# Optimization experiments

Measured on AMD Instinct MI355X. Metric: run time of the kernel, lower is better.

Reference implementation:

```python
import jax, jax.numpy as jnp
import numpy as np
from jax import lax

B, D, N, K, POOL = 256, 512, 50000, 32, 1024
ALPHA, BETA, LAMB = 1.0, 1.0, 1e-4
TAU, EPS, DELTA = 0.1, 0.1, 1e-3
SINKHORN_ITERS = 200


def matrix_sqrt(A):
    # differentiable symmetric PSD matrix sqrt via eigendecomposition
    w, v = jnp.linalg.eigh(A)
    w = jnp.clip(w, 0.0)
    return (v * jnp.sqrt(w)) @ v.T


def ridge_cov(M, delta):
    Dm = M.shape[0]
    S = M + (jnp.trace(M) / Dm * delta) * jnp.eye(Dm, dtype=M.dtype)
    return 0.5 * (S + S.T)


def sinkhorn(p, q, C, eps):
    # entropic OT, fixed-iteration Sinkhorn (ot.sinkhorn equivalent)
    Kmat = jnp.exp(-C / eps)
    def step(uv, _):
        u, v = uv
        u = p / (Kmat @ v + 1e-16)
        v = q / (Kmat.T @ u + 1e-16)
        return (u, v), None
    (u, v), _ = lax.scan(step, (jnp.ones_like(p), jnp.ones_like(q)), None, length=SINKHORN_ITERS)
    return u[:, None] * Kmat * v[None, :]


def setup_inputs():
    key = jax.random.key(0)
    k1, k2, k3, k4, k5, k6 = jax.random.split(key, 6)
    return {
        "q_batch": jax.random.normal(k1, (B, D), jnp.float32),
        "q_indices": jax.random.randint(k2, (B,), 0, POOL),
        "W": jax.random.normal(k3, (D, D), jnp.float32) * 0.05,
        "X": jax.random.normal(k4, (N, D), jnp.float32),
        "pre_indices": jax.random.randint(k5, (POOL, K), 0, N),
        "pre_weights": jax.random.uniform(k6, (POOL, K), jnp.float32, 0.1, 1.0),
    }


def _forward(q_batch, W, X, pre_weights, q_indices, pre_indices):
    T = q_batch @ W  # model := single linear layer, T_q_batch [B, D]
    # ---- distribution alignment (2-Wasserstein between Gaussians) ----
    mu_X = X.mean(0)
    Sigma_X = ridge_cov(jnp.cov(X, rowvar=False).astype(X.dtype), DELTA)
    mu_t = T.mean(0)
    Sigma_t = ridge_cov(jnp.cov(T, rowvar=False).astype(T.dtype), max(DELTA, 1e-4))
    term_mean = jnp.sum((mu_t - mu_X) ** 2)
    s_t = matrix_sqrt(Sigma_t)
    M = s_t @ Sigma_X @ s_t
    s_m = matrix_sqrt(0.5 * (M + M.T))
    term_cov = jnp.trace(Sigma_X + Sigma_t - 2.0 * s_m)
    loss_dist = term_mean + jnp.clip(term_cov, 0.0)
    # ---- kNN consistency with entropic OT ----
    T_sg = lax.stop_gradient(T)  # faiss search is on detached queries
    d2 = (T_sg ** 2).sum(1, keepdims=True) - 2.0 * T_sg @ X.T + (X ** 2).sum(1)[None, :]
    _, post_idx = lax.top_k(-d2, K)  # exact brute-force kNN == faiss IndexFlatL2
    Xn = X[post_idx]  # [B, K, D]
    l2 = ((T[:, None, :] - Xn) ** 2).sum(-1)  # [B, K], grads flow through T
    post_w = jax.nn.softmax(-l2 / TAU, axis=1)
    post_w = jnp.clip(post_w, 1e-8)
    post_w = post_w / post_w.sum(1, keepdims=True)
    pre_idx_b = pre_indices[q_indices]  # [B, K]
    pre_w = jnp.clip(pre_weights[q_indices], 1e-8)
    pre_w = pre_w / pre_w.sum(1, keepdims=True)
    # fixed-size support = concat(pre, post) of size 2K; duplicated points cost 0
    # to move between, so OT value matches the deduped-union formulation
    support = jnp.concatenate([pre_idx_b, post_idx], axis=1)  # [B, 2K]
    S = X[support]  # [B, 2K, D]
    sq = (S ** 2).sum(-1)
    C = jnp.clip(sq[:, :, None] + sq[:, None, :] - 2.0 * jnp.einsum('bid,bjd->bij', S, S), 0.0)
    med = jnp.median(C.reshape(C.shape[0], -1), axis=1)
    C = C / (med[:, None, None] + 1e-8)
    zeros = jnp.zeros_like(pre_w)
    p = jnp.concatenate([pre_w, zeros], axis=1)   # pre mass on first K slots
    q = jnp.concatenate([zeros, post_w], axis=1)  # post mass on last K slots
    plans = jax.vmap(lambda pp, qq, cc: sinkhorn(pp, qq, cc, EPS))(p, q, C)
    loss_knn = (plans * C).sum((1, 2)).mean()
    loss_reg = 0.5 * jnp.sum(W ** 2)
    total = ALPHA * loss_dist + BETA * loss_knn + LAMB * loss_reg
    return total, loss_dist, loss_knn


def reference(q_batch, q_indices, W, X, pre_indices, pre_weights):
    return _forward(q_batch, W, X, pre_weights, q_indices, pre_indices)
```

## Files before the change

### kernel.cpp

```cpp
#include <hip/hip_runtime.h>
#include <float.h>
#include <math.h>

#define BB 256
#define DD 512
#define NN 50000
#define KK 32
#define NS_ITERS 11
#define PARTS 8
#define PCH 6250

#define OFF_G     0
#define OFF_SC    262144
#define OFF_CS    262208
#define OFF_CSS   262720
#define ZERO_F    263232
#define OFF_T     263232
#define OFF_TC    394304
#define OFF_P     525376
#define OFF_H     656448
#define OFF_XSQ   723008
#define OFF_RUNI  781200
#define OFF_PW    789392
#define OFF_PRW   797584
#define OFF_D2    805776

#define OFF_UUT   (OFF_G)
#define OFF_TCTC  (OFF_G + 65536)
#define OFF_W     (OFF_G + 131072)
#define OFF_M     (OFF_G + 131328)
#define OFF_MUT   (OFF_G + 200000)

typedef __attribute__((ext_vector_type(8))) short bf16x8;
typedef __attribute__((ext_vector_type(4))) float f32x4;

__device__ __forceinline__ float waveSum(float v) {
#pragma unroll
  for (int off = 32; off > 0; off >>= 1) v += __shfl_xor(v, off);
  return v;
}

__device__ __forceinline__ void cvt_write(float4 v, unsigned short* hi, unsigned short* lo, int sa) {
  unsigned int b0 = __float_as_uint(v.x), b1 = __float_as_uint(v.y);
  unsigned int b2 = __float_as_uint(v.z), b3 = __float_as_uint(v.w);
  unsigned int h0 = b0 & 0xffff0000u, h1 = b1 & 0xffff0000u;
  unsigned int h2 = b2 & 0xffff0000u, h3 = b3 & 0xffff0000u;
  float l0 = v.x - __uint_as_float(h0), l1 = v.y - __uint_as_float(h1);
  float l2 = v.z - __uint_as_float(h2), l3 = v.w - __uint_as_float(h3);
  *(unsigned int*)&hi[sa]     = (h0 >> 16) | h1;
  *(unsigned int*)&hi[sa + 2] = (h2 >> 16) | h3;
  *(unsigned int*)&lo[sa]     = (__float_as_uint(l0) >> 16) | (__float_as_uint(l1) & 0xffff0000u);
  *(unsigned int*)&lo[sa + 2] = (__float_as_uint(l2) >> 16) | (__float_as_uint(l3) & 0xffff0000u);
}

__device__ __forceinline__ void cvt1(float x, unsigned short* hp, unsigned short* lp) {
  unsigned int bb = __float_as_uint(x);
  unsigned int hb = bb & 0xffff0000u;
  float lo = x - __uint_as_float(hb);
  *hp = (unsigned short)(hb >> 16);
  *lp = (unsigned short)(__float_as_uint(lo) >> 16);
}

__global__ void __launch_bounds__(256) k_g64_nn(const float* __restrict__ A,
                                                const float* __restrict__ B,
                                                float* __restrict__ C,
                                                int K, int lda, int ldb, int ldc, float scale,
                                                float* __restrict__ musum) {
  __shared__ float As[64][65], Bs[64][65];
  __shared__ float cp[64];
  int m0 = blockIdx.y * 64, n0 = blockIdx.x * 64;
  int t = threadIdx.x, tr = t >> 4, tc = t & 15;
  float acc[4][4] = {{0.f}};
  for (int k0 = 0; k0 < K; k0 += 64) {
#pragma unroll
    for (int p = 0; p < 16; ++p) {
      int l = t + 256 * p;
      int r = l >> 6, c = l & 63;
      As[r][c] = A[(m0 + r) * lda + k0 + c];
      Bs[r][c] = B[(k0 + r) * ldb + n0 + c];
    }
    __syncthreads();
#pragma unroll 16
    for (int kk = 0; kk < 64; ++kk) {
      float a[4], b[4];
#pragma unroll
      for (int u = 0; u < 4; ++u) a[u] = As[tr + 16 * u][kk];
#pragma unroll
      for (int v = 0; v < 4; ++v) b[v] = Bs[kk][tc + 16 * v];
#pragma unroll
      for (int u = 0; u < 4; ++u)
#pragma unroll
        for (int v = 0; v < 4; ++v) acc[u][v] += a[u] * b[v];
    }
    __syncthreads();
  }
#pragma unroll
  for (int u = 0; u < 4; ++u)
#pragma unroll
    for (int v = 0; v < 4; ++v)
      C[(m0 + tr + 16 * u) * ldc + n0 + tc + 16 * v] = acc[u][v] * scale;
  if (musum != nullptr) {
    if (t < 64) cp[t] = 0.f;
    __syncthreads();
#pragma unroll
    for (int v = 0; v < 4; ++v) {
      float s = 0.f;
#pragma unroll
      for (int u = 0; u < 4; ++u) s += acc[u][v];
      atomicAdd(&cp[tc + 16 * v], s * scale);
    }
    __syncthreads();
    if (t < 64) atomicAdd(&musum[n0 + t], cp[t]);
  }
}

__global__ void __launch_bounds__(256) k_g64_nt(const float* __restrict__ A,
                                                const float* __restrict__ B,
                                                float* __restrict__ C,
                                                int K, int lda, int ldb, int ldc, float scale) {
  __shared__ float As[64][65], Bs[64][65];
  int m0 = blockIdx.y * 64, n0 = blockIdx.x * 64;
  int t = threadIdx.x, tr = t >> 4, tc = t & 15;
  float acc[4][4] = {{0.f}};
  for (int k0 = 0; k0 < K; k0 += 64) {
#pragma unroll
    for (int p = 0; p < 16; ++p) {
      int l = t + 256 * p;
      int r = l >> 6, c = l & 63;
      As[r][c] = A[(m0 + r) * lda + k0 + c];
      Bs[r][c] = B[(n0 + r) * ldb + k0 + c];
    }
    __syncthreads();
#pragma unroll 16
    for (int kk = 0; kk < 64; ++kk) {
      float a[4], b[4];
#pragma unroll
      for (int u = 0; u < 4; ++u) a[u] = As[tr + 16 * u][kk];
#pragma unroll
      for (int v = 0; v < 4; ++v) b[v] = Bs[tc + 16 * v][kk];
#pragma unroll
      for (int u = 0; u < 4; ++u)
#pragma unroll
        for (int v = 0; v < 4; ++v) acc[u][v] += a[u] * b[v];
    }
    __syncthreads();
  }
#pragma unroll
  for (int u = 0; u < 4; ++u)
#pragma unroll
    for (int v = 0; v < 4; ++v)
      C[(m0 + tr + 16 * u) * ldc + n0 + tc + 16 * v] = acc[u][v] * scale;
}

__global__ void __launch_bounds__(256) k_vgemm(const float* __restrict__ T,
                                               const float* __restrict__ X,
                                               float* __restrict__ V,
                                               float* __restrict__ m) {
  __shared__ unsigned short Ah[128 * 72], Al[128 * 72], Bh[128 * 72], Bl[128 * 72];
  __shared__ float colpart[128];
  int bj = blockIdx.x, bi = blockIdx.y;
  int t = threadIdx.x;
  int wave = t >> 6, lane = t & 63;
  int m0 = (wave >> 1) * 64, n0 = (wave & 1) * 64;
  int lrow = lane & 15, lq = lane >> 4;
  int r_ = t >> 4, c4_ = (t & 15) * 4;
  f32x4 acc[4][4] = {};
  float4 pa[8], pb[8];
#pragma unroll
  for (int f = 0; f < 8; ++f) {
    int r = f * 16 + r_;
    pa[f] = *(const float4*)&T[(bi * 128 + r) * 512 + c4_];
    int jg = bj * 128 + r;
    float4 vb = {0.f, 0.f, 0.f, 0.f};
    if (jg < NN) vb = *(const float4*)&X[(size_t)jg * 512 + c4_];
    pb[f] = vb;
  }
  for (int kc = 0; kc < 512; kc += 64) {
#pragma unroll
    for (int f = 0; f < 8; ++f) {
      int sa = (f * 16 + r_) * 72 + c4_;
      cvt_write(pa[f], Ah, Al, sa);
      cvt_write(pb[f], Bh, Bl, sa);
    }
    __syncthreads();
    if (kc < 448) {
      int kn = kc + 64;
#pragma unroll
      for (int f = 0; f < 8; ++f) {
        int r = f * 16 + r_;
        pa[f] = *(const float4*)&T[(bi * 128 + r) * 512 + kn + c4_];
        int jg = bj * 128 + r;
        float4 vb = {0.f, 0.f, 0.f, 0.f};
        if (jg < NN) vb = *(const float4*)&X[(size_t)jg * 512 + kn + c4_];
        pb[f] = vb;
      }
    }
#pragma unroll
    for (int ks = 0; ks < 2; ++ks) {
      int kb = ks * 32 + lq * 8;
      bf16x8 ah[4], al[4], bh[4], bl[4];
#pragma unroll
      for (int mi = 0; mi < 4; ++mi) {
        int ro = (m0 + mi * 16 + lrow) * 72 + kb;
        ah[mi] = *(const bf16x8*)&Ah[ro];
        al[mi] = *(const bf16x8*)&Al[ro];
      }
#pragma unroll
      for (int nj = 0; nj < 4; ++nj) {
        int ro = (n0 + nj * 16 + lrow) * 72 + kb;
        bh[nj] = *(const bf16x8*)&Bh[ro];
        bl[nj] = *(const bf16x8*)&Bl[ro];
      }
#pragma unroll
      for (int mi = 0; mi < 4; ++mi)
#pragma unroll
        for (int nj = 0; nj < 4; ++nj) {
          acc[mi][nj] = __builtin_amdgcn_mfma_f32_16x16x32_bf16(ah[mi], bh[nj], acc[mi][nj], 0, 0, 0);
          acc[mi][nj] = __builtin_amdgcn_mfma_f32_16x16x32_bf16(ah[mi], bl[nj], acc[mi][nj], 0, 0, 0);
          acc[mi][nj] = __builtin_amdgcn_mfma_f32_16x16x32_bf16(al[mi], bh[nj], acc[mi][nj], 0, 0, 0);
        }
    }
    __syncthreads();
  }
  if (t < 128) colpart[t] = 0.f;
  __syncthreads();
#pragma unroll
  for (int mi = 0; mi < 4; ++mi)
#pragma unroll
    for (int nj = 0; nj < 4; ++nj)
#pragma unroll
      for (int r = 0; r < 4; ++r) {
        int row = bi * 128 + m0 + mi * 16 + lq * 4 + r;
        int col = bj * 128 + n0 + nj * 16 + lrow;
        if (col < NN) V[(size_t)row * NN + col] = acc[mi][nj][r];
      }
#pragma unroll
  for (int nj = 0; nj < 4; ++nj) {
    float s = 0.f;
#pragma unroll
    for (int mi = 0; mi < 4; ++mi)
#pragma unroll
      for (int r = 0; r < 4; ++r) s += acc[mi][nj][r];
    atomicAdd(&colpart[n0 + nj * 16 + lrow], s);
  }
  __syncthreads();
  if (t < 128) {
    int col = bj * 128 + t;
    if (col < NN) atomicAdd(&m[col], colpart[t] * (1.0f / 256.0f));
  }
}

__global__ void __launch_bounds__(256) k_uut(const float* __restrict__ V,
                                             const float* __restrict__ m,
                                             float* __restrict__ UUT) {
  __shared__ unsigned short Ah[128 * 72], Al[128 * 72], Bh[128 * 72], Bl[128 * 72];
  __shared__ __align__(16) float ms[1000];
  const int pi_[3] = {0, 0, 1}, pj_[3] = {0, 1, 1};
  int bi = pi_[blockIdx.x], bj = pj_[blockIdx.x];
  int j0 = blockIdx.y * 1000, jlim = j0 + 1000;
  int t = threadIdx.x;
  int wave = t >> 6, lane = t & 63;
  int m0 = (wave >> 1) * 64, n0 = (wave & 1) * 64;
  int lrow = lane & 15, lq = lane >> 4;
  int r_ = t >> 4, c4_ = (t & 15) * 4;
  f32x4 acc[4][4] = {};
  if (t < 250) ((float4*)ms)[t] = *(const float4*)&m[j0 + t * 4];
  float4 pa[8], pb[8];
#pragma unroll
  for (int f = 0; f < 8; ++f) {
    int r = f * 16 + r_;
    int jb = j0 + c4_;
    float4 va = {0.f, 0.f, 0.f, 0.f}, vb = {0.f, 0.f, 0.f, 0.f};
    if (jb < jlim) {
      va = *(const float4*)&V[(size_t)(bi * 128 + r) * NN + jb];
      vb = *(const float4*)&V[(size_t)(bj * 128 + r) * NN + jb];
    }
    pa[f] = va; pb[f] = vb;
  }
  __syncthreads();
  for (int ch = 0; ch < 16; ++ch) {
    int jc = j0 + ch * 64;
#pragma unroll
    for (int f = 0; f < 8; ++f) {
      int sa = (f * 16 + r_) * 72 + c4_;
      int jb = jc + c4_;
      float4 va = pa[f], vb = pb[f];
      if (jb < jlim) {
        float4 mm = *(const float4*)&ms[jb - j0];
        va.x -= mm.x; va.y -= mm.y; va.z -= mm.z; va.w -= mm.w;
        vb.x -= mm.x; vb.y -= mm.y; vb.z -= mm.z; vb.w -= mm.w;
      }
      cvt_write(va, Ah, Al, sa);
      cvt_write(vb, Bh, Bl, sa);
    }
    __syncthreads();
    if (ch < 15) {
      int jn = j0 + (ch + 1) * 64;
#pragma unroll
      for (int f = 0; f < 8; ++f) {
        int r = f * 16 + r_;
        int jb = jn + c4_;
        float4 va = {0.f, 0.f, 0.f, 0.f}, vb = {0.f, 0.f, 0.f, 0.f};
        if (jb < jlim) {
          va = *(const float4*)&V[(size_t)(bi * 128 + r) * NN + jb];
          vb = *(const float4*)&V[(size_t)(bj * 128 + r) * NN + jb];
        }
        pa[f] = va; pb[f] = vb;
      }
    }
#pragma unroll
    for (int ks = 0; ks < 2; ++ks) {
      int kb = ks * 32 + lq * 8;
      bf16x8 ah[4], al[4], bh[4], bl[4];
#pragma unroll
      for (int mi = 0; mi < 4; ++mi) {
        int ro = (m0 + mi * 16 + lrow) * 72 + kb;
        ah[mi] = *(const bf16x8*)&Ah[ro];
        al[mi] = *(const bf16x8*)&Al[ro];
      }
#pragma unroll
      for (int nj = 0; nj < 4; ++nj) {
        int ro = (n0 + nj * 16 + lrow) * 72 + kb;
        bh[nj] = *(const bf16x8*)&Bh[ro];
        bl[nj] = *(const bf16x8*)&Bl[ro];
      }
#pragma unroll
      for (int mi = 0; mi < 4; ++mi)
#pragma unroll
        for (int nj = 0; nj < 4; ++nj) {
          acc[mi][nj] = __builtin_amdgcn_mfma_f32_16x16x32_bf16(ah[mi], bh[nj], acc[mi][nj], 0, 0, 0);
          acc[mi][nj] = __builtin_amdgcn_mfma_f32_16x16x32_bf16(ah[mi], bl[nj], acc[mi][nj], 0, 0, 0);
          acc[mi][nj] = __builtin_amdgcn_mfma_f32_16x16x32_bf16(al[mi], bh[nj], acc[mi][nj], 0, 0, 0);
        }
    }
    __syncthreads();
  }
#pragma unroll
  for (int mi = 0; mi < 4; ++mi)
#pragma unroll
    for (int nj = 0; nj < 4; ++nj)
#pragma unroll
      for (int r = 0; r < 4; ++r) {
        int row = bi * 128 + m0 + mi * 16 + lq * 4 + r;
        int col = bj * 128 + n0 + nj * 16 + lrow;
        atomicAdd(&UUT[row * 256 + col], acc[mi][nj][r]);
      }
}

__global__ void __launch_bounds__(256) k_colstatX(const float* __restrict__ X, float* __restrict__ colsum,
                                                  float* __restrict__ colss) {
  __shared__ float shs[512], shss[512];
  int b = blockIdx.x, t = threadIdx.x;
  int c4 = (t & 127) * 4, g = t >> 7;
  int r0 = b * 200 + g;
  float sx = 0, sy = 0, sz = 0, sw = 0;
  float qx = 0, qy = 0, qz = 0, qw = 0;
#pragma unroll 4
  for (int it = 0; it < 100; ++it) {
    float4 v = *(const float4*)&X[(size_t)(r0 + 2 * it) * 512 + c4];
    sx += v.x; sy += v.y; sz += v.z; sw += v.w;
    qx += v.x * v.x; qy += v.y * v.y; qz += v.z * v.z; qw += v.w * v.w;
  }
  if (g == 1) {
    int o = (t - 128) * 4;
    shs[o] = sx; shs[o + 1] = sy; shs[o + 2] = sz; shs[o + 3] = sw;
    shss[o] = qx; shss[o + 1] = qy; shss[o + 2] = qz; shss[o + 3] = qw;
  }
  __syncthreads();
  if (g == 0) {
    int o = t * 4;
    atomicAdd(&colsum[c4],     sx + shs[o]);
    atomicAdd(&colsum[c4 + 1], sy + shs[o + 1]);
    atomicAdd(&colsum[c4 + 2], sz + shs[o + 2]);
    atomicAdd(&colsum[c4 + 3], sw + shs[o + 3]);
    atomicAdd(&colss[c4],     qx + shss[o]);
    atomicAdd(&colss[c4 + 1], qy + shss[o + 1]);
    atomicAdd(&colss[c4 + 2], qz + shss[o + 2]);
    atomicAdd(&colss[c4 + 3], qw + shss[o + 3]);
  }
}

__global__ void k_xsq(const float* __restrict__ X, float* __restrict__ xsq) {
  int row = blockIdx.x * 4 + (threadIdx.x >> 6);
  int lane = threadIdx.x & 63;
  const float* Xr = X + (size_t)row * 512;
  float s = 0.f;
#pragma unroll
  for (int d = 0; d < 8; ++d) { float v = Xr[lane + 64 * d]; s += v * v; }
  s = waveSum(s);
  if (lane == 0) xsq[row] = s;
}

__global__ void k_centerT(const float* __restrict__ T, const float* __restrict__ mu,
                          float* __restrict__ Tc, float* __restrict__ scal) {
  __shared__ float red[4];
  int t = threadIdx.x;
  int base = blockIdx.x * 1024;
  float ss = 0.f;
#pragma unroll
  for (int p = 0; p < 4; ++p) {
    int l = base + p * 256 + t;
    float v = T[l] - mu[l & 511] * (1.0f / 256.0f);
    Tc[l] = v;
    ss += v * v;
  }
  ss = waveSum(ss);
  if ((t & 63) == 0) red[t >> 6] = ss;
  __syncthreads();
  if (t == 0) atomicAdd(&scal[0], red[0] + red[1] + red[2] + red[3]);
}

__global__ void k_trCX(const float* __restrict__ colsum, const float* __restrict__ colss,
                       float* __restrict__ scal) {
  __shared__ float red[8];
  int t = threadIdx.x;
  float mu = colsum[t] * (1.0f / 50000.0f);
  float v = (colss[t] - 50000.0f * mu * mu) * (1.0f / 49999.0f);
  v = waveSum(v);
  if ((t & 63) == 0) red[t >> 6] = v;
  __syncthreads();
  if (t == 0) {
    float s = 0;
    for (int i = 0; i < 8; ++i) s += red[i];
    scal[1] = s;
  }
}

__global__ void __launch_bounds__(256) k_wvec(const float* __restrict__ T,
                                              const float* __restrict__ colsum,
                                              float* __restrict__ w, float* __restrict__ scal) {
  __shared__ float cs[512];
  int t = threadIdx.x, lane = t & 63, wv_ = t >> 6;
  cs[t] = colsum[t] * (1.0f / 50000.0f);
  cs[t + 256] = colsum[t + 256] * (1.0f / 50000.0f);
  __syncthreads();
  int rbase = blockIdx.x * 32 + wv_ * 8;
  float tot = 0.f;
  for (int rr = 0; rr < 8; ++rr) {
    int row = rbase + rr;
    float a = 0.f;
#pragma unroll
    for (int d = 0; d < 8; ++d) a += T[row * 512 + lane + 64 * d] * cs[lane + 64 * d];
    a = waveSum(a);
    if (lane == 0) { w[row] = a; tot += a; }
  }
  if (lane == 0) atomicAdd(&scal[6], tot);
}

__global__ void k_hfix(const float* __restrict__ UUT, const float* __restrict__ TcTc,
                       const float* __restrict__ w, const float* __restrict__ scal,
                       float* __restrict__ H) {
  int l = blockIdx.x * 256 + threadIdx.x;
  int i = l >> 8, j = l & 255;
  float u = (i >= 128 && j < 128) ? UUT[j * 256 + i] : UUT[i * 256 + j];
  float rho = scal[1] * (1e-3f / 512.0f);
  float wm = scal[6] * (1.0f / 256.0f);
  float wi = w[i] - wm, wj = w[j] - wm;
  H[l] = (u - 50000.0f * wi * wj) * (1.0f / (49999.0f * 255.0f))
       + rho * TcTc[i * 256 + j] * (1.0f / 255.0f);
}

__global__ void __launch_bounds__(256) k_power(const float* __restrict__ H,
                                               float* __restrict__ scal) {
  __shared__ float v[256], nv[256], red[4];
  int t = threadIdx.x;
  float rt = scal[0] * (1.0f / 255.0f) * (1e-3f / 512.0f);
  v[t] = 1.0f;
  __syncthreads();
  float n2 = 256.0f, n3 = 256.0f;
  for (int it = 0; it < 3; ++it) {
    float s = rt * v[t];
    for (int j = 0; j < 256; ++j) s += H[j * 256 + t] * v[j];
    nv[t] = s;
    float ss = waveSum(s * s);
    if ((t & 63) == 0) red[t >> 6] = ss;
    __syncthreads();
    float norm2 = red[0] + red[1] + red[2] + red[3];
    if (it == 1) n2 = norm2;
    if (it == 2) n3 = norm2;
    v[t] = nv[t];
    __syncthreads();
  }
  float d = H[t * 256 + t] + rt;
#pragma unroll
  for (int off = 32; off > 0; off >>= 1) d = fmaxf(d, __shfl_xor(d, off));
  if ((t & 63) == 0) red[t >> 6] = d;
  __syncthreads();
  if (t == 0) {
    float lam = sqrtf(n3 / n2);
    float md = fmaxf(fmaxf(red[0], red[1]), fmaxf(red[2], red[3]));
    scal[5] = fmaxf(1.3f * lam, md);
  }
}

__global__ void k_nsinit(const float* __restrict__ H, const float* __restrict__ scal,
                         float* __restrict__ Y, float* __restrict__ Z) {
  int l = blockIdx.x * 256 + threadIdx.x;
  int i = l >> 8, j = l & 255;
  float rt = scal[0] * (1.0f / 255.0f) * (1e-3f / 512.0f);
  float inv = 1.0f / scal[5];
  Y[l] = (H[l] + ((i == j) ? rt : 0.f)) * inv;
  Z[l] = (i == j) ? 1.0f : 0.f;
}

__global__ void __launch_bounds__(256) k_nsp(const float* __restrict__ Z,
                                             const float* __restrict__ Y,
                                             float* __restrict__ P) {
  __shared__ unsigned short Ah[64 * 72], Al[64 * 72], Bh[64 * 72], Bl[64 * 72];
  int n0b = blockIdx.x * 64, m0b = blockIdx.y * 64;
  int t = threadIdx.x, wave = t >> 6, lane = t & 63;
  int m0 = (wave >> 1) * 32, n0 = (wave & 1) * 32;
  int lrow = lane & 15, lq = lane >> 4;
  f32x4 acc[2][2] = {};
  for (int k0 = 0; k0 < 256; k0 += 64) {
#pragma unroll
    for (int f = 0; f < 4; ++f) {
      int lin = f * 256 + t;
      int r = lin >> 4, c4 = (lin & 15) * 4;
      float4 va = *(const float4*)&Z[(m0b + r) * 256 + k0 + c4];
      cvt_write(va, Ah, Al, r * 72 + c4);
      float4 vb = *(const float4*)&Y[(k0 + r) * 256 + n0b + c4];
      cvt1(vb.x, &Bh[(c4 + 0) * 72 + r], &Bl[(c4 + 0) * 72 + r]);
      cvt1(vb.y, &Bh[(c4 + 1) * 72 + r], &Bl[(c4 + 1) * 72 + r]);
      cvt1(vb.z, &Bh[(c4 + 2) * 72 + r], &Bl[(c4 + 2) * 72 + r]);
      cvt1(vb.w, &Bh[(c4 + 3) * 72 + r], &Bl[(c4 + 3) * 72 + r]);
    }
    __syncthreads();
#pragma unroll
    for (int ks = 0; ks < 2; ++ks) {
      int kb = ks * 32 + lq * 8;
      bf16x8 ah[2], al2[2], bh[2], bl2[2];
#pragma unroll
      for (int mi = 0; mi < 2; ++mi) {
        int ro = (m0 + mi * 16 + lrow) * 72 + kb;
        ah[mi] = *(const bf16x8*)&Ah[ro];
        al2[mi] = *(const bf16x8*)&Al[ro];
      }
#pragma unroll
      for (int nj = 0; nj < 2; ++nj) {
        int ro = (n0 + nj * 16 + lrow) * 72 + kb;
        bh[nj] = *(const bf16x8*)&Bh[ro];
        bl2[nj] = *(const bf16x8*)&Bl[ro];
      }
#pragma unroll
      for (int mi = 0; mi < 2; ++mi)
#pragma unroll
        for (int nj = 0; nj < 2; ++nj) {
          acc[mi][nj] = __builtin_amdgcn_mfma_f32_16x16x32_bf16(ah[mi], bh[nj], acc[mi][nj], 0, 0, 0);
          acc[mi][nj] = __builtin_amdgcn_mfma_f32_16x16x32_bf16(ah[mi], bl2[nj], acc[mi][nj], 0, 0, 0);
          acc[mi][nj] = __builtin_amdgcn_mfma_f32_16x16x32_bf16(al2[mi], bh[nj], acc[mi][nj], 0, 0, 0);
        }
    }
    __syncthreads();
  }
#pragma unroll
  for (int mi = 0; mi < 2; ++mi)
#pragma unroll
    for (int nj = 0; nj < 2; ++nj)
#pragma unroll
      for (int r = 0; r < 4; ++r) {
        int row = m0b + m0 + mi * 16 + lq * 4 + r;
        int col = n0b + n0 + nj * 16 + lrow;
        P[row * 256 + col] = acc[mi][nj][r];
      }
}

__global__ void __launch_bounds__(256) k_nsu(const float* __restrict__ Y, const float* __restrict__ Z,
                                             const float* __restrict__ Pm,
                                             float* __restrict__ Yn, float* __restrict__ Zn) {
  __shared__ unsigned short Ah[64 * 72], Al[64 * 72], Bh[64 * 72], Bl[64 * 72];
  int zz = blockIdx.z;
  const float* A = zz ? Pm : Y;
  const float* B = zz ? Z : Pm;
  const float* D = zz ? Z : Y;
  float* O = zz ? Zn : Yn;
  int n0b = blockIdx.x * 64, m0b = blockIdx.y * 64;
  int t = threadIdx.x, wave = t >> 6, lane = t & 63;
  int m0 = (wave >> 1) * 32, n0 = (wave & 1) * 32;
  int lrow = lane & 15, lq = lane >> 4;
  f32x4 acc[2][2] = {};
  for (int k0 = 0; k0 < 256; k0 += 64) {
#pragma unroll
    for (int f = 0; f < 4; ++f) {
      int lin = f * 256 + t;
      int r = lin >> 4, c4 = (lin & 15) * 4;
      float4 va = *(const float4*)&A[(m0b + r) * 256 + k0 + c4];
      cvt_write(va, Ah, Al, r * 72 + c4);
      float4 vb = *(const float4*)&B[(k0 + r) * 256 + n0b + c4];
      cvt1(vb.x, &Bh[(c4 + 0) * 72 + r], &Bl[(c4 + 0) * 72 + r]);
      cvt1(vb.y, &Bh[(c4 + 1) * 72 + r], &Bl[(c4 + 1) * 72 + r]);
      cvt1(vb.z, &Bh[(c4 + 2) * 72 + r], &Bl[(c4 + 2) * 72 + r]);
      cvt1(vb.w, &Bh[(c4 + 3) * 72 + r], &Bl[(c4 + 3) * 72 + r]);
    }
    __syncthreads();
#pragma unroll
    for (int ks = 0; ks < 2; ++ks) {
      int kb = ks * 32 + lq * 8;
      bf16x8 ah[2], al2[2], bh[2], bl2[2];
#pragma unroll
      for (int mi = 0; mi < 2; ++mi) {
        int ro = (m0 + mi * 16 + lrow) * 72 + kb;
        ah[mi] = *(const bf16x8*)&Ah[ro];
        al2[mi] = *(const bf16x8*)&Al[ro];
      }
#pragma unroll
      for (int nj = 0; nj < 2; ++nj) {
        int ro = (n0 + nj * 16 + lrow) * 72 + kb;
        bh[nj] = *(const bf16x8*)&Bh[ro];
        bl2[nj] = *(const bf16x8*)&Bl[ro];
      }
#pragma unroll
      for (int mi = 0; mi < 2; ++mi)
#pragma unroll
        for (int nj = 0; nj < 2; ++nj) {
          acc[mi][nj] = __builtin_amdgcn_mfma_f32_16x16x32_bf16(ah[mi], bh[nj], acc[mi][nj], 0, 0, 0);
          acc[mi][nj] = __builtin_amdgcn_mfma_f32_16x16x32_bf16(ah[mi], bl2[nj], acc[mi][nj], 0, 0, 0);
          acc[mi][nj] = __builtin_amdgcn_mfma_f32_16x16x32_bf16(al2[mi], bh[nj], acc[mi][nj], 0, 0, 0);
        }
    }
    __syncthreads();
  }
#pragma unroll
  for (int mi = 0; mi < 2; ++mi)
#pragma unroll
    for (int nj = 0; nj < 2; ++nj)
#pragma unroll
      for (int r = 0; r < 4; ++r) {
        int row = m0b + m0 + mi * 16 + lq * 4 + r;
        int col = n0b + n0 + nj * 16 + lrow;
        int idx = row * 256 + col;
        O[idx] = 1.5f * D[idx] - 0.5f * acc[mi][nj][r];
      }
}

__global__ void k_ns_trace(const float* __restrict__ Y, float* __restrict__ scal) {
  __shared__ float red[4];
  int t = threadIdx.x;
  float v = Y[t * 256 + t];
  v = waveSum(v);
  if ((t & 63) == 0) red[t >> 6] = v;
  __syncthreads();
  if (t == 0) {
    float tr = red[0] + red[1] + red[2] + red[3];
    float rt = scal[0] * (1.0f / 255.0f) * (1e-3f / 512.0f);
    scal[2] = sqrtf(scal[5]) * tr + 256.0f * sqrtf(rt);
  }
}

__global__ void __launch_bounds__(256) k_topk_part(const float* __restrict__ V,
                                                   const float* __restrict__ xsq,
                                                   float* __restrict__ candv,
                                                   int* __restrict__ candi) {
  __shared__ float bufv[512];
  __shared__ int bufi[512];
  __shared__ int lcount;
  __shared__ float tvs;
  __shared__ int tis;
  int part = blockIdx.x, q = blockIdx.y, t = threadIdx.x;
  int base = part * PCH;
  int lane = t & 63;
  if (t == 0) { lcount = 0; tvs = FLT_MAX; tis = 0x7fffffff; }
  __syncthreads();
  const float* rowV = V + (size_t)q * NN + base;
  const float* xs = xsq + base;

  auto flush = [&]() {
    __syncthreads();
    int c = lcount;
    for (int s = c + t; s < 512; s += 256) { bufv[s] = FLT_MAX; bufi[s] = 0x7fffffff; }
    __syncthreads();
    for (int ssz = 2; ssz <= 512; ssz <<= 1) {
      for (int st = ssz >> 1; st > 0; st >>= 1) {
        int i = 2 * t - (t & (st - 1));
        int j = i + st;
        bool up = ((i & ssz) == 0);
        float a = bufv[i], b = bufv[j];
        int ai = bufi[i], bi2 = bufi[j];
        bool agtb = (a > b) || (a == b && ai > bi2);
        if (agtb == up) { bufv[i] = b; bufv[j] = a; bufi[i] = bi2; bufi[j] = ai; }
        __syncthreads();
      }
    }
    if (t == 0) { lcount = 32; tvs = bufv[31]; tis = bufi[31]; }
    __syncthreads();
  };

  int ntile = (PCH + 255) >> 8;
  for (int tile = 0; tile < ntile; ++tile) {
    int j = tile * 256 + t;
    float val = 0.f; int idx = 0;
    bool pred = false;
    if (j < PCH) {
      val = xs[j] - 2.0f * rowV[j];
      idx = base + j;
      float tv = tvs; int ti = tis;
      pred = (val < tv) || (val == tv && idx < ti);
    }
    unsigned long long mask = __ballot(pred);
    if (mask) {
      int lead = __ffsll((unsigned long long)mask) - 1;
      int cnt = __popcll(mask);
      int basep = 0;
      if (lane == lead) basep = atomicAdd(&lcount, cnt);
      basep = __shfl(basep, lead);
      if (pred) {
        int off = __popcll(mask & ((1ull << lane) - 1ull));
        int slot = basep + off;
        bufv[slot] = val; bufi[slot] = idx;
      }
    }
    __syncthreads();
    if (lcount >= 256) flush();
  }
  flush();
  if (t < 32) {
    candv[(q * PARTS + part) * 32 + t] = bufv[t];
    candi[(q * PARTS + part) * 32 + t] = bufi[t];
  }
}

__global__ void __launch_bounds__(128) k_topk_final(const float* __restrict__ candv,
                                                    const int* __restrict__ candi,
                                                    int* __restrict__ runi) {
  __shared__ float v[256];
  __shared__ int ix[256];
  int q = blockIdx.x, t = threadIdx.x;
  v[t] = candv[q * 256 + t];
  v[t + 128] = candv[q * 256 + t + 128];
  ix[t] = candi[q * 256 + t];
  ix[t + 128] = candi[q * 256 + t + 128];
  __syncthreads();
  for (int ssz = 2; ssz <= 256; ssz <<= 1) {
    for (int st = ssz >> 1; st > 0; st >>= 1) {
      int i = 2 * t - (t & (st - 1));
      int j = i + st;
      bool up = ((i & ssz) == 0);
      float a = v[i], b = v[j];
      int ai = ix[i], bi = ix[j];
      bool agtb = (a > b) || (a == b && ai > bi);
      if (agtb == up) { v[i] = b; v[j] = a; ix[i] = bi; ix[j] = ai; }
      __syncthreads();
    }
  }
  if (t < 32) runi[q * 32 + t] = ix[t];
}

__global__ void __launch_bounds__(64) k_l2soft(const float* __restrict__ T, const float* __restrict__ X,
                                               const int* __restrict__ runi, const int* __restrict__ qidx,
                                               const float* __restrict__ prew, float* __restrict__ postw,
                                               float* __restrict__ prewn) {
  __shared__ float l2s[32];
  int b = blockIdx.x, lane = threadIdx.x;
  int qi = qidx[b];
  float pwv = (lane < 32) ? fmaxf(prew[qi * 32 + lane], 1e-8f) : 0.f;
  float psum = waveSum(pwv);
  if (lane < 32) prewn[b * 32 + lane] = pwv / psum;
  const float* Tb = T + b * 512;
  for (int n = 0; n < 32; ++n) {
    int nb = runi[b * 32 + n];
    const float* Xr = X + (size_t)nb * 512;
    float acc = 0.f;
#pragma unroll
    for (int d = 0; d < 8; ++d) {
      float df = Tb[lane + 64 * d] - Xr[lane + 64 * d];
      acc += df * df;
    }
    acc = waveSum(acc);
    if (lane == 0) l2s[n] = acc;
  }
  __syncthreads();
  float lg = (lane < 32) ? (-l2s[lane] * 10.0f) : -FLT_MAX;
  float mx = lg;
#pragma unroll
  for (int off = 32; off > 0; off >>= 1) mx = fmaxf(mx, __shfl_xor(mx, off));
  float e = (lane < 32) ? expf(lg - mx) : 0.f;
  float es = waveSum(e);
  float wv = e / es;
  wv = fmaxf(wv, 1e-8f);
  float ws2 = (lane < 32) ? wv : 0.f;
  ws2 = waveSum(ws2);
  if (lane < 32) postw[b * 32 + lane] = wv / ws2;
}

__global__ void __launch_bounds__(256) k_batch(const float* __restrict__ X, const int* __restrict__ qidx,
                                               const int* __restrict__ pre_idx, const int* __restrict__ runi,
                                               const float* __restrict__ prewn, const float* __restrict__ postw,
                                               float* __restrict__ scal) {
  __shared__ float G[64][65];
  __shared__ float Cm[64][65];
  __shared__ unsigned short Ah[64 * 72], Al[64 * 72];
  __shared__ int supp[64];
  __shared__ float uuS[32], vvS[32];
  __shared__ float red[4];
  __shared__ float medsh;
  __shared__ unsigned int hist[256];
  __shared__ unsigned int wtot[4];
  __shared__ unsigned int selp;
  __shared__ int selk;
  __shared__ unsigned int cw[4], mw[4];
  int b = blockIdx.x, t = threadIdx.x;
  int wave = t >> 6, lane = t & 63;
  if (t < 32) supp[t] = pre_idx[qidx[b] * 32 + t];
  else if (t < 64) supp[t] = runi[b * 32 + t - 32];
  if (t == 0) { selp = 0u; selk = 992; }
  __syncthreads();
  {
    int m0 = (wave >> 1) * 32, n0 = (wave & 1) * 32;
    int lrow = lane & 15, lq = lane >> 4;
    int r_ = t >> 4, c4_ = (t & 15) * 4;
    f32x4 acc[2][2] = {};
    float4 pf[4];
#pragma unroll
    for (int f = 0; f < 4; ++f) {
      int r = f * 16 + r_;
      pf[f] = *(const float4*)&X[(size_t)supp[r] * 512 + c4_];
    }
    for (int kc = 0; kc < 512; kc += 64) {
#pragma unroll
      for (int f = 0; f < 4; ++f)
        cvt_write(pf[f], Ah, Al, (f * 16 + r_) * 72 + c4_);
      __syncthreads();
      if (kc < 448) {
        int kn = kc + 64;
#pragma unroll
        for (int f = 0; f < 4; ++f) {
          int r = f * 16 + r_;
          pf[f] = *(const float4*)&X[(size_t)supp[r] * 512 + kn + c4_];
        }
      }
#pragma unroll
      for (int ks = 0; ks < 2; ++ks) {
        int kb = ks * 32 + lq * 8;
        bf16x8 ah[2], al[2], bh[2], bl[2];
#pragma unroll
        for (int mi = 0; mi < 2; ++mi) {
          int ro = (m0 + mi * 16 + lrow) * 72 + kb;
          ah[mi] = *(const bf16x8*)&Ah[ro];
          al[mi] = *(const bf16x8*)&Al[ro];
        }
#pragma unroll
        for (int nj = 0; nj < 2; ++nj) {
          int ro = (n0 + nj * 16 + lrow) * 72 + kb;
          bh[nj] = *(const bf16x8*)&Ah[ro];
          bl[nj] = *(const bf16x8*)&Al[ro];
        }
#pragma unroll
        for (int mi = 0; mi < 2; ++mi)
#pragma unroll
          for (int nj = 0; nj < 2; ++nj) {
            acc[mi][nj] = __builtin_amdgcn_mfma_f32_16x16x32_bf16(ah[mi], bh[nj], acc[mi][nj], 0, 0, 0);
            acc[mi][nj] = __builtin_amdgcn_mfma_f32_16x16x32_bf16(ah[mi], bl[nj], acc[mi][nj], 0, 0, 0);
            acc[mi][nj] = __builtin_amdgcn_mfma_f32_16x16x32_bf16(al[mi], bh[nj], acc[mi][nj], 0, 0, 0);
          }
      }
      __syncthreads();
    }
#pragma unroll
    for (int mi = 0; mi < 2; ++mi)
#pragma unroll
      for (int nj = 0; nj < 2; ++nj)
#pragma unroll
        for (int r = 0; r < 4; ++r)
          G[m0 + mi * 16 + lq * 4 + r][n0 + nj * 16 + lrow] = acc[mi][nj][r];
  }
  __syncthreads();
  for (int l = t; l < 4096; l += 256) {
    int i = l >> 6, j = l & 63;
    Cm[i][j] = fmaxf(G[i][i] + G[j][j] - 2.0f * G[i][j], 0.f);
  }
  __syncthreads();
  for (int pass = 0; pass < 4; ++pass) {
    int shift = 24 - 8 * pass;
    hist[t] = 0u;
    __syncthreads();
    for (int l = t; l < 4096; l += 256) {
      int i = l >> 6, j = l & 63;
      if (i < j) {
        unsigned int u = __float_as_uint(Cm[i][j]) & 0x7fffffffu;
        bool match = (pass == 0) || (((u ^ selp) >> (shift + 8)) == 0u);
        if (match) atomicAdd(&hist[(u >> shift) & 255], 1u);
      }
    }
    __syncthreads();
    unsigned int h = hist[t];
    unsigned int c = h;
#pragma unroll
    for (int off = 1; off < 64; off <<= 1) {
      unsigned int n = __shfl_up(c, off);
      if ((t & 63) >= off) c += n;
    }
    if ((t & 63) == 63) wtot[t >> 6] = c;
    __syncthreads();
    unsigned int offw = 0;
    for (int w2 = 0; w2 < (t >> 6); ++w2) offw += wtot[w2];
    c += offw;
    int k = selk;
    if ((int)c >= k && (int)(c - h) < k) {
      selk = k - (int)(c - h);
      selp = selp | ((unsigned int)t << shift);
    }
    __syncthreads();
  }
  {
    unsigned int target = selp;
    unsigned int cnt = 0, mn = 0xffffffffu;
    for (int l = t; l < 4096; l += 256) {
      int i = l >> 6, j = l & 63;
      if (i < j) {
        unsigned int u = __float_as_uint(Cm[i][j]) & 0x7fffffffu;
        if (u <= target) cnt++;
        else mn = (u < mn) ? u : mn;
      }
    }
#pragma unroll
    for (int off = 32; off > 0; off >>= 1) {
      cnt += __shfl_xor(cnt, off);
      unsigned int m2 = __shfl_xor(mn, off);
      mn = (m2 < mn) ? m2 : mn;
    }
    if (lane == 0) { cw[wave] = cnt; mw[wave] = mn; }
    __syncthreads();
    if (t == 0) {
      unsigned int ct = cw[0] + cw[1] + cw[2] + cw[3];
      unsigned int mt = mw[0];
      mt = (mw[1] < mt) ? mw[1] : mt;
      mt = (mw[2] < mt) ? mw[2] : mt;
      mt = (mw[3] < mt) ? mw[3] : mt;
      float v992 = __uint_as_float(target);
      float v993 = (ct >= 993u) ? v992 : __uint_as_float(mt);
      medsh = 0.5f * (v992 + v993) + 1e-8f;
    }
    __syncthreads();
  }
  float inv = 1.0f / medsh;
  for (int l = t; l < 4096; l += 256) {
    int i = l >> 6, j = l & 63;
    float cn = Cm[i][j] * inv;
    Cm[i][j] = cn;
    G[i][j] = expf(-cn * 10.0f);
  }
  __syncthreads();
  if (wave == 0) {
    int half = lane >> 5;
    int l = lane & 31;
    int cb = half * 16;
    float p_l = prewn[b * 32 + l];
    float q_l = postw[b * 32 + l];
    float Kr16[16], Kt16[16];
#pragma unroll
    for (int c2 = 0; c2 < 16; ++c2) Kr16[c2] = G[l][32 + cb + c2];
#pragma unroll
    for (int r2 = 0; r2 < 16; ++r2) Kt16[r2] = G[cb + r2][32 + l];
    float r0 = 0.f;
#pragma unroll
    for (int c2 = 0; c2 < 32; ++c2) r0 += G[l][half * 32 + c2];
    r0 += __shfl_xor(r0, 32);
    float u = p_l / (r0 + 1e-16f);
    float s0 = 0.f, s1 = 0.f, s2 = 0.f, s3 = 0.f;
#pragma unroll
    for (int r2 = 0; r2 < 16; r2 += 4) {
      s0 += Kt16[r2]     * __shfl(u, cb + r2);
      s1 += Kt16[r2 + 1] * __shfl(u, cb + r2 + 1);
      s2 += Kt16[r2 + 2] * __shfl(u, cb + r2 + 2);
      s3 += Kt16[r2 + 3] * __shfl(u, cb + r2 + 3);
    }
    float sv = (s0 + s1) + (s2 + s3);
    sv += __shfl_xor(sv, 32);
    float v = q_l / (sv + 1e-16f);
    for (int it = 1; it < 200; ++it) {
      float uprev = u, vprev = v;
      float a0 = 0.f, a1 = 0.f, a2 = 0.f, a3 = 0.f;
#pragma unroll
      for (int c2 = 0; c2 < 16; c2 += 4) {
        a0 += Kr16[c2]     * __shfl(v, cb + c2);
        a1 += Kr16[c2 + 1] * __shfl(v, cb + c2 + 1);
        a2 += Kr16[c2 + 2] * __shfl(v, cb + c2 + 2);
        a3 += Kr16[c2 + 3] * __shfl(v, cb + c2 + 3);
      }
      float au = (a0 + a1) + (a2 + a3);
      au += __shfl_xor(au, 32);
      u = p_l / (au + 1e-16f);
      a0 = 0.f; a1 = 0.f; a2 = 0.f; a3 = 0.f;
#pragma unroll
      for (int r2 = 0; r2 < 16; r2 += 4) {
        a0 += Kt16[r2]     * __shfl(u, cb + r2);
        a1 += Kt16[r2 + 1] * __shfl(u, cb + r2 + 1);
        a2 += Kt16[r2 + 2] * __shfl(u, cb + r2 + 2);
        a3 += Kt16[r2 + 3] * __shfl(u, cb + r2 + 3);
      }
      float bv = (a0 + a1) + (a2 + a3);
      bv += __shfl_xor(bv, 32);
      v = q_l / (bv + 1e-16f);
      if (__all(u == uprev && v == vprev)) break;
    }
    if (t < 32) { uuS[t] = u; vvS[t] = v; }
  }
  __syncthreads();
  float lacc = 0.f;
#pragma unroll
  for (int q8 = 0; q8 < 4; ++q8) {
    int l = q8 * 256 + t;
    int i = l >> 5, j = l & 31;
    lacc += uuS[i] * G[i][32 + j] * vvS[j] * Cm[i][32 + j];
  }
  lacc = waveSum(lacc);
  if ((t & 63) == 0) red[t >> 6] = lacc;
  __syncthreads();
  if (t == 0)
    atomicAdd(&scal[3], (red[0] + red[1] + red[2] + red[3]) * (1.0f / 256.0f));
}

__global__ void k_wreg(const float* __restrict__ W, float* __restrict__ scal) {
  __shared__ float red[4];
  int t = threadIdx.x;
  int base = blockIdx.x * 2048;
  float ss = 0.f;
#pragma unroll
  for (int p = 0; p < 8; ++p) {
    float v = W[base + p * 256 + t];
    ss += v * v;
  }
  ss = waveSum(ss);
  if ((t & 63) == 0) red[t >> 6] = ss;
  __syncthreads();
  if (t == 0) atomicAdd(&scal[4], red[0] + red[1] + red[2] + red[3]);
}

__global__ void k_combine(const float* __restrict__ mu_t, const float* __restrict__ colsum,
                          const float* __restrict__ scal, float* __restrict__ out) {
  __shared__ float red[8];
  int t = threadIdx.x;
  float dm = mu_t[t] * (1.0f / 256.0f) - colsum[t] * (1.0f / 50000.0f);
  float v = dm * dm;
  v = waveSum(v);
  if ((t & 63) == 0) red[t >> 6] = v;
  __syncthreads();
  if (t == 0) {
    float term_mean = 0.f;
    for (int i = 0; i < 8; ++i) term_mean += red[i];
    float trCT = scal[0] * (1.0f / 255.0f);
    float trCX = scal[1];
    float S = scal[2];
    float term_cov = trCX * 1.001f + trCT * 1.001f - 2.0f * S;
    term_cov = fmaxf(term_cov, 0.f);
    float loss_dist = term_mean + term_cov;
    float loss_knn = scal[3];
    float loss_reg = 0.5f * scal[4];
    out[0] = loss_dist + loss_knn + 1e-4f * loss_reg;
    out[1] = loss_dist;
    out[2] = loss_knn;
  }
}

extern "C" void kernel_launch(void* const* d_in, const int* in_sizes, int n_in,
                              void* d_out, int out_size, void* d_ws, size_t ws_size,
                              hipStream_t stream) {
  const float* q = (const float*)d_in[0];
  const int* qidx = (const int*)d_in[1];
  const float* W = (const float*)d_in[2];
  const float* X = (const float*)d_in[3];
  const int* pre_idx = (const int*)d_in[4];
  const float* prew = (const float*)d_in[5];
  float* out = (float*)d_out;
  float* ws = (float*)d_ws;

  float* scal = ws + OFF_SC;
  float* colsum = ws + OFF_CS;
  float* colss = ws + OFF_CSS;
  float* T = ws + OFF_T;
  float* Tc = ws + OFF_TC;
  float* H = ws + OFF_H;
  float* mu_t = ws + OFF_MUT;
  float* xsq = ws + OFF_XSQ;
  int* runi = (int*)(ws + OFF_RUNI);
  float* postw = ws + OFF_PW;
  float* prewn = ws + OFF_PRW;
  float* V = ws + OFF_D2;
  float* UUT = ws + OFF_UUT;
  float* TcTc = ws + OFF_TCTC;
  float* wv = ws + OFF_W;
  float* m = ws + OFF_M;
  float* candv = ws + OFF_P;
  int* candi = (int*)(ws + OFF_P + 65536);

  hipMemsetAsync(d_ws, 0, (size_t)ZERO_F * 4, stream);

  k_g64_nn<<<dim3(8, 4), 256, 0, stream>>>(q, W, T, 512, 512, 512, 512, 1.0f, mu_t);
  k_colstatX<<<250, 256, 0, stream>>>(X, colsum, colss);
  k_xsq<<<12500, 256, 0, stream>>>(X, xsq);
  k_centerT<<<128, 256, 0, stream>>>(T, mu_t, Tc, scal);
  k_trCX<<<1, 512, 0, stream>>>(colsum, colss, scal);
  k_vgemm<<<dim3(391, 2), 256, 0, stream>>>(T, X, V, m);
  k_topk_part<<<dim3(PARTS, 256), 256, 0, stream>>>(V, xsq, candv, candi);
  k_topk_final<<<256, 128, 0, stream>>>(candv, candi, runi);
  k_g64_nt<<<dim3(4, 4), 256, 0, stream>>>(Tc, Tc, TcTc, 512, 512, 512, 256, 1.0f);
  k_wvec<<<8, 256, 0, stream>>>(T, colsum, wv, scal);
  k_uut<<<dim3(3, 50), 256, 0, stream>>>(V, m, UUT);
  k_hfix<<<256, 256, 0, stream>>>(UUT, TcTc, wv, scal, H);
  {
    float* Y = ws + OFF_TC;
    float* Z = ws + OFF_TC + 65536;
    float* Y2 = ws + OFF_P;
    float* Z2 = ws + OFF_P + 65536;
    float* Pm = ws + OFF_G;
    k_power<<<1, 256, 0, stream>>>(H, scal);
    k_nsinit<<<256, 256, 0, stream>>>(H, scal, Y, Z);
    for (int it = 0; it < NS_ITERS; ++it) {
      k_nsp<<<dim3(4, 4), 256, 0, stream>>>(Z, Y, Pm);
      k_nsu<<<dim3(4, 4, 2), 256, 0, stream>>>(Y, Z, Pm, Y2, Z2);
      float* tmp = Y; Y = Y2; Y2 = tmp;
      tmp = Z; Z = Z2; Z2 = tmp;
    }
    k_ns_trace<<<1, 256, 0, stream>>>(Y, scal);
  }
  k_l2soft<<<256, 64, 0, stream>>>(T, X, runi, qidx, prew, postw, prewn);
  k_batch<<<256, 256, 0, stream>>>(X, qidx, pre_idx, runi, prewn, postw, scal);
  k_wreg<<<128, 256, 0, stream>>>(W, scal);
  k_combine<<<1, 512, 0, stream>>>(mu_t, colsum, scal, out);
}
```

Before: 925.1 us.

## Fuse row-norm into column stats, parallelize l2soft, bitwise median, period-2 Sinkhorn exit

```diff
diff --git a/kernel.cpp b/kernel.cpp
--- a/kernel.cpp
+++ b/kernel.cpp
@@ -348,47 +348,40 @@
 }
 
 __global__ void __launch_bounds__(256) k_colstatX(const float* __restrict__ X, float* __restrict__ colsum,
-                                                  float* __restrict__ colss) {
-  __shared__ float shs[512], shss[512];
+                                                  float* __restrict__ colss, float* __restrict__ xsq) {
+  __shared__ float shs[512], shq[512];
   int b = blockIdx.x, t = threadIdx.x;
-  int c4 = (t & 127) * 4, g = t >> 7;
-  int r0 = b * 200 + g;
-  float sx = 0, sy = 0, sz = 0, sw = 0;
-  float qx = 0, qy = 0, qz = 0, qw = 0;
-#pragma unroll 4
-  for (int it = 0; it < 100; ++it) {
-    float4 v = *(const float4*)&X[(size_t)(r0 + 2 * it) * 512 + c4];
-    sx += v.x; sy += v.y; sz += v.z; sw += v.w;
-    qx += v.x * v.x; qy += v.y * v.y; qz += v.z * v.z; qw += v.w * v.w;
-  }
-  if (g == 1) {
-    int o = (t - 128) * 4;
-    shs[o] = sx; shs[o + 1] = sy; shs[o + 2] = sz; shs[o + 3] = sw;
-    shss[o] = qx; shss[o + 1] = qy; shss[o + 2] = qz; shss[o + 3] = qw;
-  }
-  __syncthreads();
-  if (g == 0) {
-    int o = t * 4;
-    atomicAdd(&colsum[c4],     sx + shs[o]);
-    atomicAdd(&colsum[c4 + 1], sy + shs[o + 1]);
-    atomicAdd(&colsum[c4 + 2], sz + shs[o + 2]);
-    atomicAdd(&colsum[c4 + 3], sw + shs[o + 3]);
-    atomicAdd(&colss[c4],     qx + shss[o]);
-    atomicAdd(&colss[c4 + 1], qy + shss[o + 1]);
-    atomicAdd(&colss[c4 + 2], qz + shss[o + 2]);
-    atomicAdd(&colss[c4 + 3], qw + shss[o + 3]);
-  }
-}
-
-__global__ void k_xsq(const float* __restrict__ X, float* __restrict__ xsq) {
-  int row = blockIdx.x * 4 + (threadIdx.x >> 6);
-  int lane = threadIdx.x & 63;
-  const float* Xr = X + (size_t)row * 512;
-  float s = 0.f;
-#pragma unroll
-  for (int d = 0; d < 8; ++d) { float v = Xr[lane + 64 * d]; s += v * v; }
-  s = waveSum(s);
-  if (lane == 0) xsq[row] = s;
+  int wave = t >> 6, lane = t & 63;
+  shs[t] = 0.f; shq[t] = 0.f; shs[t + 256] = 0.f; shq[t + 256] = 0.f;
+  __syncthreads();
+  int c0 = lane * 4;
+  float s0 = 0, s1 = 0, s2 = 0, s3 = 0, s4 = 0, s5 = 0, s6 = 0, s7 = 0;
+  float q0 = 0, q1 = 0, q2 = 0, q3 = 0, q4 = 0, q5 = 0, q6 = 0, q7 = 0;
+  int r0 = b * 200 + wave * 50;
+  for (int rr = 0; rr < 50; ++rr) {
+    const float* Xr = X + (size_t)(r0 + rr) * 512;
+    float4 a = *(const float4*)&Xr[c0];
+    float4 c = *(const float4*)&Xr[c0 + 256];
+    s0 += a.x; s1 += a.y; s2 += a.z; s3 += a.w;
+    s4 += c.x; s5 += c.y; s6 += c.z; s7 += c.w;
+    float ax = a.x * a.x, ay = a.y * a.y, az = a.z * a.z, aw = a.w * a.w;
+    float cx = c.x * c.x, cy = c.y * c.y, cz = c.z * c.z, cw = c.w * c.w;
+    q0 += ax; q1 += ay; q2 += az; q3 += aw;
+    q4 += cx; q5 += cy; q6 += cz; q7 += cw;
+    float rsq = waveSum(((ax + ay) + (az + aw)) + ((cx + cy) + (cz + cw)));
+    if (lane == 0) xsq[r0 + rr] = rsq;
+  }
+  atomicAdd(&shs[c0 + 0], s0); atomicAdd(&shs[c0 + 1], s1);
+  atomicAdd(&shs[c0 + 2], s2); atomicAdd(&shs[c0 + 3], s3);
+  atomicAdd(&shs[c0 + 256], s4); atomicAdd(&shs[c0 + 257], s5);
+  atomicAdd(&shs[c0 + 258], s6); atomicAdd(&shs[c0 + 259], s7);
+  atomicAdd(&shq[c0 + 0], q0); atomicAdd(&shq[c0 + 1], q1);
+  atomicAdd(&shq[c0 + 2], q2); atomicAdd(&shq[c0 + 3], q3);
+  atomicAdd(&shq[c0 + 256], q4); atomicAdd(&shq[c0 + 257], q5);
+  atomicAdd(&shq[c0 + 258], q6); atomicAdd(&shq[c0 + 259], q7);
+  __syncthreads();
+  atomicAdd(&colsum[t], shs[t]);             atomicAdd(&colss[t], shq[t]);
+  atomicAdd(&colsum[t + 256], shs[t + 256]); atomicAdd(&colss[t + 256], shq[t + 256]);
 }
 
 __global__ void k_centerT(const float* __restrict__ T, const float* __restrict__ mu,
@@ -745,18 +738,23 @@
   if (t < 32) runi[q * 32 + t] = ix[t];
 }
 
-__global__ void __launch_bounds__(64) k_l2soft(const float* __restrict__ T, const float* __restrict__ X,
-                                               const int* __restrict__ runi, const int* __restrict__ qidx,
-                                               const float* __restrict__ prew, float* __restrict__ postw,
-                                               float* __restrict__ prewn) {
+__global__ void __launch_bounds__(256) k_l2soft(const float* __restrict__ T, const float* __restrict__ X,
+                                                const int* __restrict__ runi, const int* __restrict__ qidx,
+                                                const float* __restrict__ prew, float* __restrict__ postw,
+                                                float* __restrict__ prewn) {
   __shared__ float l2s[32];
-  int b = blockIdx.x, lane = threadIdx.x;
+  int b = blockIdx.x, t = threadIdx.x;
+  int wave = t >> 6, lane = t & 63;
   int qi = qidx[b];
-  float pwv = (lane < 32) ? fmaxf(prew[qi * 32 + lane], 1e-8f) : 0.f;
-  float psum = waveSum(pwv);
-  if (lane < 32) prewn[b * 32 + lane] = pwv / psum;
+  if (wave == 0) {
+    float pwv = (lane < 32) ? fmaxf(prew[qi * 32 + lane], 1e-8f) : 0.f;
+    float psum = waveSum(pwv);
+    if (lane < 32) prewn[b * 32 + lane] = pwv / psum;
+  }
   const float* Tb = T + b * 512;
-  for (int n = 0; n < 32; ++n) {
+#pragma unroll
+  for (int n8 = 0; n8 < 8; ++n8) {
+    int n = wave * 8 + n8;
     int nb = runi[b * 32 + n];
     const float* Xr = X + (size_t)nb * 512;
     float acc = 0.f;
@@ -769,17 +767,19 @@
     if (lane == 0) l2s[n] = acc;
   }
   __syncthreads();
-  float lg = (lane < 32) ? (-l2s[lane] * 10.0f) : -FLT_MAX;
-  float mx = lg;
-#pragma unroll
-  for (int off = 32; off > 0; off >>= 1) mx = fmaxf(mx, __shfl_xor(mx, off));
-  float e = (lane < 32) ? expf(lg - mx) : 0.f;
-  float es = waveSum(e);
-  float wv = e / es;
-  wv = fmaxf(wv, 1e-8f);
-  float ws2 = (lane < 32) ? wv : 0.f;
-  ws2 = waveSum(ws2);
-  if (lane < 32) postw[b * 32 + lane] = wv / ws2;
+  if (wave == 0) {
+    float lg = (lane < 32) ? (-l2s[lane] * 10.0f) : -FLT_MAX;
+    float mx = lg;
+#pragma unroll
+    for (int off = 32; off > 0; off >>= 1) mx = fmaxf(mx, __shfl_xor(mx, off));
+    float e = (lane < 32) ? expf(lg - mx) : 0.f;
+    float es = waveSum(e);
+    float wv = e / es;
+    wv = fmaxf(wv, 1e-8f);
+    float ws2 = (lane < 32) ? wv : 0.f;
+    ws2 = waveSum(ws2);
+    if (lane < 32) postw[b * 32 + lane] = wv / ws2;
+  }
 }
 
 __global__ void __launch_bounds__(256) k_batch(const float* __restrict__ X, const int* __restrict__ qidx,
@@ -793,16 +793,11 @@
   __shared__ float uuS[32], vvS[32];
   __shared__ float red[4];
   __shared__ float medsh;
-  __shared__ unsigned int hist[256];
-  __shared__ unsigned int wtot[4];
-  __shared__ unsigned int selp;
-  __shared__ int selk;
   __shared__ unsigned int cw[4], mw[4];
   int b = blockIdx.x, t = threadIdx.x;
   int wave = t >> 6, lane = t & 63;
   if (t < 32) supp[t] = pre_idx[qidx[b] * 32 + t];
   else if (t < 64) supp[t] = runi[b * 32 + t - 32];
-  if (t == 0) { selp = 0u; selk = 992; }
   __syncthreads();
   {
     int m0 = (wave >> 1) * 32, n0 = (wave & 1) * 32;
@@ -864,53 +859,36 @@
           G[m0 + mi * 16 + lq * 4 + r][n0 + nj * 16 + lrow] = acc[mi][nj][r];
   }
   __syncthreads();
-  for (int l = t; l < 4096; l += 256) {
+  unsigned int uval[16];
+#pragma unroll
+  for (int s = 0; s < 16; ++s) {
+    int l = s * 256 + t;
     int i = l >> 6, j = l & 63;
-    Cm[i][j] = fmaxf(G[i][i] + G[j][j] - 2.0f * G[i][j], 0.f);
-  }
-  __syncthreads();
-  for (int pass = 0; pass < 4; ++pass) {
-    int shift = 24 - 8 * pass;
-    hist[t] = 0u;
-    __syncthreads();
-    for (int l = t; l < 4096; l += 256) {
-      int i = l >> 6, j = l & 63;
-      if (i < j) {
-        unsigned int u = __float_as_uint(Cm[i][j]) & 0x7fffffffu;
-        bool match = (pass == 0) || (((u ^ selp) >> (shift + 8)) == 0u);
-        if (match) atomicAdd(&hist[(u >> shift) & 255], 1u);
-      }
-    }
-    __syncthreads();
-    unsigned int h = hist[t];
-    unsigned int c = h;
-#pragma unroll
-    for (int off = 1; off < 64; off <<= 1) {
-      unsigned int n = __shfl_up(c, off);
-      if ((t & 63) >= off) c += n;
-    }
-    if ((t & 63) == 63) wtot[t >> 6] = c;
-    __syncthreads();
-    unsigned int offw = 0;
-    for (int w2 = 0; w2 < (t >> 6); ++w2) offw += wtot[w2];
-    c += offw;
-    int k = selk;
-    if ((int)c >= k && (int)(c - h) < k) {
-      selk = k - (int)(c - h);
-      selp = selp | ((unsigned int)t << shift);
-    }
-    __syncthreads();
+    float cc = fmaxf(G[i][i] + G[j][j] - 2.0f * G[i][j], 0.f);
+    Cm[i][j] = cc;
+    uval[s] = (i < j) ? (__float_as_uint(cc) & 0x7fffffffu) : 0xffffffffu;
+  }
+  unsigned int ans = 0;
+  for (int bb = 30; bb >= 0; --bb) {
+    unsigned int test = ans | (1u << bb);
+    int cw_ = 0;
+#pragma unroll
+    for (int s = 0; s < 16; ++s)
+      cw_ += __popcll(__ballot(uval[s] < test));
+    __syncthreads();
+    if (lane == 0) red[wave] = (float)cw_;
+    __syncthreads();
+    int cnt = (int)(red[0] + red[1] + red[2] + red[3]);
+    if (cnt < 992) ans = test;
   }
   {
-    unsigned int target = selp;
+    unsigned int target = ans;
     unsigned int cnt = 0, mn = 0xffffffffu;
-    for (int l = t; l < 4096; l += 256) {
-      int i = l >> 6, j = l & 63;
-      if (i < j) {
-        unsigned int u = __float_as_uint(Cm[i][j]) & 0x7fffffffu;
-        if (u <= target) cnt++;
-        else mn = (u < mn) ? u : mn;
-      }
+#pragma unroll
+    for (int s = 0; s < 16; ++s) {
+      unsigned int u = uval[s];
+      if (u <= target) cnt++;
+      else mn = (u < mn) ? u : mn;
     }
 #pragma unroll
     for (int off = 32; off > 0; off >>= 1) {
@@ -918,6 +896,7 @@
       unsigned int m2 = __shfl_xor(mn, off);
       mn = (m2 < mn) ? m2 : mn;
     }
+    __syncthreads();
     if (lane == 0) { cw[wave] = cnt; mw[wave] = mn; }
     __syncthreads();
     if (t == 0) {
@@ -967,8 +946,9 @@
     float sv = (s0 + s1) + (s2 + s3);
     sv += __shfl_xor(sv, 32);
     float v = q_l / (sv + 1e-16f);
+    float pu = u, pv = v;
+    float ppu = 0.f, ppv = 0.f;
     for (int it = 1; it < 200; ++it) {
-      float uprev = u, vprev = v;
       float a0 = 0.f, a1 = 0.f, a2 = 0.f, a3 = 0.f;
 #pragma unroll
       for (int c2 = 0; c2 < 16; c2 += 4) {
@@ -991,7 +971,12 @@
       float bv = (a0 + a1) + (a2 + a3);
       bv += __shfl_xor(bv, 32);
       v = q_l / (bv + 1e-16f);
-      if (__all(u == uprev && v == vprev)) break;
+      if (__all(u == pu && v == pv)) break;
+      if (it >= 2 && __all(u == ppu && v == ppv)) {
+        if ((199 - it) & 1) { u = pu; v = pv; }
+        break;
+      }
+      ppu = pu; ppv = pv; pu = u; pv = v;
     }
     if (t < 32) { uuS[t] = u; vvS[t] = v; }
   }
@@ -1086,8 +1071,7 @@
   hipMemsetAsync(d_ws, 0, (size_t)ZERO_F * 4, stream);
 
   k_g64_nn<<<dim3(8, 4), 256, 0, stream>>>(q, W, T, 512, 512, 512, 512, 1.0f, mu_t);
-  k_colstatX<<<250, 256, 0, stream>>>(X, colsum, colss);
-  k_xsq<<<12500, 256, 0, stream>>>(X, xsq);
+  k_colstatX<<<250, 256, 0, stream>>>(X, colsum, colss, xsq);
   k_centerT<<<128, 256, 0, stream>>>(T, mu_t, Tc, scal);
   k_trCX<<<1, 512, 0, stream>>>(colsum, colss, scal);
   k_vgemm<<<dim3(391, 2), 256, 0, stream>>>(T, X, V, m);
@@ -1113,7 +1097,7 @@
     }
     k_ns_trace<<<1, 256, 0, stream>>>(Y, scal);
   }
-  k_l2soft<<<256, 64, 0, stream>>>(T, X, runi, qidx, prew, postw, prewn);
+  k_l2soft<<<256, 256, 0, stream>>>(T, X, runi, qidx, prew, postw, prewn);
   k_batch<<<256, 256, 0, stream>>>(X, qidx, pre_idx, runi, prewn, postw, scal);
   k_wreg<<<128, 256, 0, stream>>>(W, scal);
   k_combine<<<1, 512, 0, stream>>>(mu_t, colsum, scal, out);
```

Result: faster. 905.3 us (-2.1%).
